# Kernel optimization log

Measured on AMD Instinct MI355X. Metric: run time of the kernel, lower is better.

## Reference

```python
import jax, jax.numpy as jnp
import numpy as np

N_NODES = 50000
C = 128
E = 800000
B = 4096
NEG = 5
NUM_LAYERS = 3


def setup_inputs() -> dict:
    key = jax.random.key(0)
    ks = jax.random.split(key, 8)
    edge_index = jax.random.randint(ks[0], (2, E), 0, N_NODES, dtype=jnp.int64)
    edge_weight = jax.random.uniform(ks[1], (E,), dtype=jnp.float32)
    n_id = jax.random.randint(ks[2], ((2 + NEG) * B,), 0, N_NODES, dtype=jnp.int64)
    x = jnp.zeros((1,), jnp.float32)  # ignored by forward (overwritten by id_embed)
    id_embed = jax.random.normal(ks[3], (N_NODES, C), jnp.float32) * 0.1
    w1 = jax.random.normal(ks[4], (2 * C, C), jnp.float32) * (1.0 / np.sqrt(2 * C))
    b1 = jnp.zeros((C,), jnp.float32)
    w2 = jax.random.normal(ks[5], (C, 1), jnp.float32) * (1.0 / np.sqrt(C))
    b2 = jnp.zeros((1,), jnp.float32)
    return {"x": x, "edge_index": edge_index, "edge_weight": edge_weight,
            "n_id": n_id, "neg_sample_num": NEG, "id_embed": id_embed,
            "w1": w1, "b1": b1, "w2": w2, "b2": b2}


def reference(x, edge_index, edge_weight, n_id, neg_sample_num, id_embed, w1, b1, w2, b2):
    n_nodes = id_embed.shape[0]
    row, col = edge_index[0], edge_index[1]
    # symmetric GCN normalization (LGCConv)
    deg = jax.ops.segment_sum(jnp.ones_like(row, dtype=id_embed.dtype), row,
                              num_segments=n_nodes)
    dinv = jnp.where(deg > 0, jax.lax.rsqrt(jnp.maximum(deg, 1e-12)), 0.0)
    norm = (dinv[row] * dinv[col])[:, None]  # [E,1]
    h = id_embed
    final = id_embed
    for _ in range(NUM_LAYERS):
        h = jax.ops.segment_sum(norm * h[col], row, num_segments=n_nodes)
        final = final + h
    final = final / (NUM_LAYERS + 1)
    # split n_id into (out, pos, neg) index groups
    b = n_id.shape[0] // (2 + neg_sample_num)
    out = final[n_id[:b]]
    pos = final[n_id[b:2 * b]]
    neg = final[n_id[2 * b:]]
    tiled_out = jnp.repeat(out, neg_sample_num, axis=0)  # [b*neg, C]

    def pred_head(z):  # Linear -> LeakyReLU(0.2) -> (Dropout eval=identity) -> Linear
        z = jax.nn.leaky_relu(z @ w1 + b1, negative_slope=0.2)
        return z @ w2 + b2

    pos_logit = pred_head(jnp.concatenate([out, pos], axis=-1))
    neg_logits = pred_head(jnp.concatenate([tiled_out, neg], axis=-1))
    return pos_logit, neg_logits
```

## Files before the change

### kernel.cpp

```cpp
#include <hip/hip_runtime.h>
#include <hip/hip_bf16.h>

#define C 128
#define NBKT 128
#define BCAP 8192

typedef __bf16 bf16x8 __attribute__((ext_vector_type(8)));
typedef float floatx4 __attribute__((ext_vector_type(4)));

__device__ __forceinline__ unsigned short f2bf(float f) {
    unsigned u = __float_as_uint(f);
    unsigned r = (u + 0x7FFFu + ((u >> 16) & 1u)) >> 16;
    return (unsigned short)r;
}
__device__ __forceinline__ float bflo(unsigned v) { return __uint_as_float(v << 16); }
__device__ __forceinline__ float bfhi(unsigned v) { return __uint_as_float(v & 0xFFFF0000u); }
__device__ __forceinline__ unsigned packbf(float lo, float hi) {
    return (unsigned)f2bf(lo) | ((unsigned)f2bf(hi) << 16);
}

__device__ __forceinline__ int g_idx(const void* p, long long i, int is64) {
    if (is64) return (int)((const long long*)p)[i];
    return ((const int*)p)[i];
}
__device__ __forceinline__ float g_flt(const void* p, long long i, int isf32) {
    if (isf32) return ((const float*)p)[i];
    return __uint_as_float(((unsigned)((const unsigned short*)p)[i]) << 16);
}

__global__ void k_detect(const void* edge, const void* nid, const void* emb, int* flags,
                         unsigned* g0, unsigned* g1, unsigned* g2, int* bucketcnt,
                         int N, int SST) {
    int t = threadIdx.x;
    int buf = t >> 6, w = t & 63;
    size_t o = (size_t)(w >> 5) * SST + (size_t)N * 32 + (w & 31);
    if (buf == 0) g0[o] = 0;
    else if (buf == 1) g1[o] = 0;
    else g2[o] = 0;
    if (t < NBKT) bucketcnt[t] = 0;
    if (t < 64) {
        const unsigned* wrd = (const unsigned*)edge;
        const unsigned* nw = (const unsigned*)nid;
        int predA = (t < 32) ? (wrd[2 * t + 1] == 0u) : 1;
        int predB = (t < 32) ? (nw[2 * t + 1] == 0u) : 1;
        const unsigned short* h = (const unsigned short*)emb;
        int ex = (h[2 * t] >> 7) & 0xFF;
        int plaus = (ex >= 0x6C && ex <= 0x7F) ? 1 : 0;
        unsigned long long mA = __ballot(predA);
        unsigned long long mB = __ballot(predB);
        unsigned long long mP = __ballot(plaus);
        if (t == 0) {
            flags[0] = (mA == ~0ull) ? 1 : 0;
            flags[1] = (mB == ~0ull) ? 1 : 0;
            flags[2] = (__popcll(mP) < 32) ? 1 : 0;
        }
    }
}

__global__ void k_bucketA(const void* edge, int E, int rpb, const int* flags,
                          unsigned* __restrict__ bucketbuf, int* __restrict__ bucketcnt) {
    __shared__ int lcnt[NBKT];
    __shared__ int lbase[NBKT];
    int t = threadIdx.x;
    int is64 = flags[0];
    const int PER = 8;
    int chunkSz = blockDim.x * PER;
    long long stride = (long long)gridDim.x * chunkSz;
    for (long long base = (long long)blockIdx.x * chunkSz; base < E; base += stride) {
        if (t < NBKT) lcnt[t] = 0;
        __syncthreads();
        int bkt[PER], rank[PER];
        unsigned enc[PER];
        long long e0 = base + (long long)t * PER;
        int rr[PER], cc[PER];
        if (e0 + PER <= E) {
            if (is64) {
                const long long* pr = (const long long*)edge + e0;
                const long long* pc = (const long long*)edge + E + e0;
#pragma unroll
                for (int j = 0; j < PER; j += 2) {
                    longlong2 vr = *(const longlong2*)(pr + j);
                    longlong2 vc = *(const longlong2*)(pc + j);
                    rr[j] = (int)vr.x; rr[j + 1] = (int)vr.y;
                    cc[j] = (int)vc.x; cc[j + 1] = (int)vc.y;
                }
            } else {
                const int* pr = (const int*)edge + e0;
                const int* pc = (const int*)edge + E + e0;
#pragma unroll
                for (int j = 0; j < PER; j += 4) {
                    int4 vr = *(const int4*)(pr + j);
                    int4 vc = *(const int4*)(pc + j);
                    rr[j] = vr.x; rr[j + 1] = vr.y; rr[j + 2] = vr.z; rr[j + 3] = vr.w;
                    cc[j] = vc.x; cc[j + 1] = vc.y; cc[j + 2] = vc.z; cc[j + 3] = vc.w;
                }
            }
#pragma unroll
            for (int j = 0; j < PER; ++j) {
                int b = rr[j] / rpb;
                bkt[j] = b;
                enc[j] = ((unsigned)(rr[j] - b * rpb) << 16) | (unsigned)(cc[j] & 0xFFFF);
                rank[j] = atomicAdd(&lcnt[b], 1);
            }
        } else {
#pragma unroll
            for (int j = 0; j < PER; ++j) {
                long long e = e0 + j;
                if (e < E) {
                    int r = g_idx(edge, e, is64);
                    int c = g_idx(edge, (long long)E + e, is64);
                    int b = r / rpb;
                    bkt[j] = b;
                    enc[j] = ((unsigned)(r - b * rpb) << 16) | (unsigned)(c & 0xFFFF);
                    rank[j] = atomicAdd(&lcnt[b], 1);
                } else bkt[j] = -1;
            }
        }
        __syncthreads();
        if (t < NBKT) lbase[t] = atomicAdd(&bucketcnt[t], lcnt[t]);
        __syncthreads();
#pragma unroll
        for (int j = 0; j < PER; ++j) {
            if (bkt[j] >= 0) {
                int pos = lbase[bkt[j]] + rank[j];
                if (pos < BCAP)
                    bucketbuf[(size_t)bkt[j] * BCAP + pos] = enc[j];
            }
        }
    }
}

__global__ __launch_bounds__(512) void k_bsort(
        const unsigned* __restrict__ bucketbuf, const int* __restrict__ bucketcnt,
        int* __restrict__ rowptr, float* __restrict__ dinv, float* __restrict__ di2,
        float* __restrict__ rdinv, unsigned short* __restrict__ cols16, int N, int rpb) {
    __shared__ int hist[512];
    int b = blockIdx.x;
    int t = threadIdx.x;
    int base = 0, cnt = 0, total = 0;
    for (int i = 0; i < NBKT; ++i) {
        int v = bucketcnt[i];
        if (v > BCAP) v = BCAP;
        if (i < b) base += v;
        if (i == b) cnt = v;
        total += v;
    }
    int r0 = b * rpb;
    int rows = N - r0;
    if (rows > rpb) rows = rpb;
    if (rows < 0) rows = 0;

    hist[t] = 0;
    __syncthreads();
    const unsigned* buf = bucketbuf + (size_t)b * BCAP;
    for (int i = t; i < cnt; i += 512) atomicAdd(&hist[buf[i] >> 16], 1);
    __syncthreads();
    int v = hist[t];
    __syncthreads();
    for (int off = 1; off < 512; off <<= 1) {
        int x = (t >= off) ? hist[t - off] : 0;
        __syncthreads();
        hist[t] += x;
        __syncthreads();
    }
    int excl = hist[t] - v;
    if (t < rows) {
        int r = r0 + t;
        rowptr[r] = base + excl;
        float fd = (float)v;
        float dv = (v > 0) ? rsqrtf(fd) : 0.0f;
        dinv[r] = dv;
        di2[r] = dv * dv;
        rdinv[r] = (v > 0) ? sqrtf(fd) : 0.0f;
    }
    if (b == NBKT - 1 && t == 0) rowptr[N] = total;
    __syncthreads();
    hist[t] = base + excl;
    __syncthreads();
    for (int i = t; i < cnt; i += 512) {
        unsigned u = buf[i];
        int pos = atomicAdd(&hist[u >> 16], 1);
        cols16[pos] = (unsigned short)(u & 0xFFFF);
    }
}

__global__ void k_initprep(const void* emb, const float* __restrict__ dinv,
                           unsigned* __restrict__ h0, unsigned* __restrict__ g0,
                           int n2, int SST,
                           const void* w1, const void* b1, const void* w2, const void* b2,
                           unsigned short* __restrict__ w1t, float* __restrict__ b1f,
                           float* __restrict__ w2f, float* __restrict__ b2f, const int* flags) {
    int i = blockIdx.x * blockDim.x + threadIdx.x;
    int f32 = flags[2];
    if (i < n2) {
        float lo = g_flt(emb, 2LL * i, f32);
        float hi = g_flt(emb, 2LL * i + 1, f32);
        int n = i >> 6, w = i & 63;
        size_t o = (size_t)(w >> 5) * SST + (size_t)n * 32 + (w & 31);
        h0[o] = packbf(lo, hi);
        float dv = dinv[n];
        g0[o] = packbf(lo * dv, hi * dv);
    }
    if (i < 256 * 128) {
        int k = i >> 7, n = i & 127;
        w1t[n * 256 + k] = f2bf(g_flt(w1, i, f32));
    }
    if (i < 128) {
        b1f[i] = g_flt(b1, i, f32);
        w2f[i] = g_flt(w2, i, f32);
    }
    if (i == 0) b2f[0] = g_flt(b2, 0, f32);
}

__global__ void k_layer(const int* __restrict__ rowptr, const unsigned short* __restrict__ cols16,
                        const uint4* __restrict__ gin, uint4* __restrict__ gout,
                        const float* __restrict__ di2, int N, int SSTU4) {
    int slice = blockIdx.x & 1;
    int node = (blockIdx.x >> 1) * 32 + (threadIdx.x >> 3);
    if (node >= N) return;
    int l8 = threadIdx.x & 7;
    const uint4* gs = gin + (size_t)slice * SSTU4;
    int p = rowptr[node];
    int end = rowptr[node + 1];
    float a0 = 0.f, a1 = 0.f, a2 = 0.f, a3 = 0.f;
    float a4 = 0.f, a5 = 0.f, a6 = 0.f, a7 = 0.f;
    for (int base = p; base < end; base += 8) {
        int c[8];
#pragma unroll
        for (int j = 0; j < 8; ++j) {
            int idx = base + j;
            int cv = cols16[idx];
            c[j] = (idx < end) ? cv : N;
        }
#pragma unroll
        for (int j = 0; j < 8; ++j) {
            uint4 v = gs[(size_t)c[j] * 8 + l8];
            a0 += bflo(v.x); a1 += bfhi(v.x);
            a2 += bflo(v.y); a3 += bfhi(v.y);
            a4 += bflo(v.z); a5 += bfhi(v.z);
            a6 += bflo(v.w); a7 += bfhi(v.w);
        }
    }
    float s = di2[node];
    uint4 o;
    o.x = packbf(a0 * s, a1 * s);
    o.y = packbf(a2 * s, a3 * s);
    o.z = packbf(a4 * s, a5 * s);
    o.w = packbf(a6 * s, a7 * s);
    gout[(size_t)slice * SSTU4 + (size_t)node * 8 + l8] = o;
}

__global__ void k_layer3(const int* __restrict__ rowptr, const unsigned short* __restrict__ cols16,
                         const uint4* __restrict__ gin , const uint4* __restrict__ h0,
                         const uint4* __restrict__ g1, uint4* __restrict__ fin,
                         const float* __restrict__ di2, const float* __restrict__ rdinv,
                         int N, int SSTU4) {
    int slice = blockIdx.x & 1;
    int node = (blockIdx.x >> 1) * 32 + (threadIdx.x >> 3);
    if (node >= N) return;
    int l8 = threadIdx.x & 7;
    size_t sb = (size_t)slice * SSTU4;
    const uint4* gs = gin + sb;
    int p = rowptr[node];
    int end = rowptr[node + 1];
    float a0 = 0.f, a1 = 0.f, a2 = 0.f, a3 = 0.f;
    float a4 = 0.f, a5 = 0.f, a6 = 0.f, a7 = 0.f;
    for (int base = p; base < end; base += 8) {
        int c[8];
#pragma unroll
        for (int j = 0; j < 8; ++j) {
            int idx = base + j;
            int cv = cols16[idx];
            c[j] = (idx < end) ? cv : N;
        }
#pragma unroll
        for (int j = 0; j < 8; ++j) {
            uint4 v = gs[(size_t)c[j] * 8 + l8];
            a0 += bflo(v.x); a1 += bfhi(v.x);
            a2 += bflo(v.y); a3 += bfhi(v.y);
            a4 += bflo(v.z); a5 += bfhi(v.z);
            a6 += bflo(v.w); a7 += bfhi(v.w);
        }
    }
    float s = di2[node];
    float rd = rdinv[node];
    size_t ro = (size_t)node * 8 + l8;
    uint4 x0 = h0[sb + ro];
    uint4 x1 = g1[sb + ro];
    uint4 x2 = gs[ro];
    uint4 o;
    o.x = packbf(0.25f * (bflo(x0.x) + rd * (bflo(x1.x) + bflo(x2.x) + s * a0)),
                 0.25f * (bfhi(x0.x) + rd * (bfhi(x1.x) + bfhi(x2.x) + s * a1)));
    o.y = packbf(0.25f * (bflo(x0.y) + rd * (bflo(x1.y) + bflo(x2.y) + s * a2)),
                 0.25f * (bfhi(x0.y) + rd * (bfhi(x1.y) + bfhi(x2.y) + s * a3)));
    o.z = packbf(0.25f * (bflo(x0.z) + rd * (bflo(x1.z) + bflo(x2.z) + s * a4)),
                 0.25f * (bfhi(x0.z) + rd * (bfhi(x1.z) + bfhi(x2.z) + s * a5)));
    o.w = packbf(0.25f * (bflo(x0.w) + rd * (bflo(x1.w) + bflo(x2.w) + s * a6)),
                 0.25f * (bfhi(x0.w) + rd * (bfhi(x1.w) + bfhi(x2.w) + s * a7)));
    fin[(size_t)node * 16 + slice * 8 + l8] = o;
}

__global__ void k_head(const uint4* __restrict__ fin, const void* n_id,
                       const unsigned short* __restrict__ w1t,
                       const float* __restrict__ b1f, const float* __restrict__ w2f,
                       const float* __restrict__ b2f,
                       float* __restrict__ out, int B, int NEG, const int* flags) {
    __shared__ unsigned short z[64][264];
    int t = threadIdx.x;
    int id64 = flags[1];
    int mbase = blockIdx.x * 64;

#pragma unroll
    for (int i = 0; i < 8; ++i) {
        int flat = i * 256 + t;
        int m = flat >> 5;
        int q = flat & 31;
        int gm = mbase + m;
        int r;
        if (gm < B) {
            r = (q < 16) ? g_idx(n_id, gm, id64) : g_idx(n_id, B + gm, id64);
        } else {
            int j = gm - B;
            r = (q < 16) ? g_idx(n_id, j / NEG, id64) : g_idx(n_id, 2 * B + j, id64);
        }
        uint4 v = fin[(size_t)r * 16 + (q & 15)];
        *(uint4*)((char*)&z[m][0] + q * 16) = v;
    }
    __syncthreads();

    int wave = t >> 6, lane = t & 63;
    int quad = lane >> 4, l16 = lane & 15;

    floatx4 acc[8] = {};
    bf16x8 a[8];
    const unsigned short* zrow = &z[wave * 16 + l16][0];
#pragma unroll
    for (int ks = 0; ks < 8; ++ks)
        a[ks] = *(const bf16x8*)(zrow + ks * 32 + quad * 8);

#pragma unroll
    for (int ks = 0; ks < 8; ++ks) {
#pragma unroll
        for (int nt = 0; nt < 8; ++nt) {
            bf16x8 b = *(const bf16x8*)(w1t + (nt * 16 + l16) * 256 + ks * 32 + quad * 8);
            acc[nt] = __builtin_amdgcn_mfma_f32_16x16x32_bf16(a[ks], b, acc[nt], 0, 0, 0);
        }
    }

    float s0 = 0.f, s1 = 0.f, s2 = 0.f, s3 = 0.f;
#pragma unroll
    for (int nt = 0; nt < 8; ++nt) {
        int col = nt * 16 + l16;
        float bb = b1f[col], ww = w2f[col];
        float v0 = acc[nt][0] + bb; v0 = (v0 > 0.f) ? v0 : 0.2f * v0; s0 += v0 * ww;
        float v1 = acc[nt][1] + bb; v1 = (v1 > 0.f) ? v1 : 0.2f * v1; s1 += v1 * ww;
        float v2 = acc[nt][2] + bb; v2 = (v2 > 0.f) ? v2 : 0.2f * v2; s2 += v2 * ww;
        float v3 = acc[nt][3] + bb; v3 = (v3 > 0.f) ? v3 : 0.2f * v3; s3 += v3 * ww;
    }
#pragma unroll
    for (int off = 1; off <= 8; off <<= 1) {
        s0 += __shfl_xor(s0, off, 64);
        s1 += __shfl_xor(s1, off, 64);
        s2 += __shfl_xor(s2, off, 64);
        s3 += __shfl_xor(s3, off, 64);
    }
    if (l16 == 0) {
        int rowbase = mbase + wave * 16 + quad * 4;
        float bb2 = b2f[0];
        out[rowbase + 0] = s0 + bb2;
        out[rowbase + 1] = s1 + bb2;
        out[rowbase + 2] = s2 + bb2;
        out[rowbase + 3] = s3 + bb2;
    }
}

extern "C" void kernel_launch(void* const* d_in, const int* in_sizes, int n_in,
                              void* d_out, int out_size, void* d_ws, size_t ws_size,
                              hipStream_t stream) {
    const void* edge_index = d_in[1];
    const void* n_id       = d_in[3];
    const void* id_embed   = d_in[5];
    const void* w1 = d_in[6];
    const void* b1 = d_in[7];
    const void* w2 = d_in[8];
    const void* b2 = d_in[9];
    float* out = (float*)d_out;

    const int E  = in_sizes[1] / 2;
    const int N  = in_sizes[5] / C;
    const int NEG = 5;
    const int B  = in_sizes[3] / (2 + NEG);
    const int n_out_rows = B + B * NEG;
    const int SST = (N + 1) * 32;
    const int SSTU4 = (N + 1) * 8;
    const int NB = 2 * SST;
    const int rpb = (N + NBKT - 1) / NBKT;

    size_t off = 0;
    auto alloc = [&](size_t nf) {
        char* p = (char*)d_ws + off * 4;
        off += (nf + 255) & ~(size_t)255;
        return p;
    };
    int*   flags     = (int*)alloc(8);
    int*   bucketcnt = (int*)alloc(NBKT);
    float* dinv      = (float*)alloc(N);
    float* di2       = (float*)alloc(N);
    float* rdinv     = (float*)alloc(N);
    int*   rowptr    = (int*)alloc(N + 1);
    unsigned short* cols16 = (unsigned short*)alloc(((size_t)E + 16 + 1) / 2);
    unsigned* bucketbuf = (unsigned*)alloc((size_t)NBKT * BCAP);
    unsigned* h0     = (unsigned*)alloc(NB);
    unsigned* g0     = (unsigned*)alloc(NB);
    unsigned* g1     = (unsigned*)alloc(NB);
    unsigned* g2     = (unsigned*)alloc(NB);
    unsigned* fin    = (unsigned*)alloc((size_t)N * 64);
    unsigned short* w1t = (unsigned short*)alloc(256 * 128 / 2);
    float* b1f       = (float*)alloc(C);
    float* w2f       = (float*)alloc(C);
    float* b2f       = (float*)alloc(8);

    const int BS = 256;
    k_detect<<<1, 192, 0, stream>>>(edge_index, n_id, id_embed, flags, g0, g1, g2,
                                    bucketcnt, N, SST);
    const int gridA = (E + BS * 8 - 1) / (BS * 8);
    k_bucketA<<<gridA, BS, 0, stream>>>(edge_index, E, rpb, flags, bucketbuf, bucketcnt);
    k_bsort<<<NBKT, 512, 0, stream>>>(bucketbuf, bucketcnt, rowptr, dinv, di2, rdinv,
                                      cols16, N, rpb);
    k_initprep<<<(N * 64 + BS - 1) / BS, BS, 0, stream>>>(
        id_embed, dinv, h0, g0, N * 64, SST, w1, b1, w2, b2, w1t, b1f, w2f, b2f, flags);

    const int layer_grid = ((N + 31) / 32) * 2;
    k_layer<<<layer_grid, BS, 0, stream>>>(rowptr, cols16, (const uint4*)g0, (uint4*)g1,
                                           di2, N, SSTU4);
    k_layer<<<layer_grid, BS, 0, stream>>>(rowptr, cols16, (const uint4*)g1, (uint4*)g2,
                                           di2, N, SSTU4);
    k_layer3<<<layer_grid, BS, 0, stream>>>(rowptr, cols16, (const uint4*)g2, (const uint4*)h0,
                                            (const uint4*)g1, (uint4*)fin, di2, rdinv,
                                            N, SSTU4);

    k_head<<<n_out_rows / 64, BS, 0, stream>>>((const uint4*)fin, n_id, w1t, b1f, w2f, b2f,
                                               out, B, NEG, flags);
}
```

Measured before the change: 216.0 us.

## Fuse init and three propagation layers into a cooperative persistent kernel

Replaces the separate init-prep and three per-layer launches with one cooperative persistent kernel that uses grid-wide syncs between phases, with a multi-launch fallback. The first layer now applies the per-column dinv scale inside the gather instead of storing a pre-scaled g0, so g0 is gone. Features move from a two-slice layout to a contiguous 256-byte row, gathered by 16 lanes per node. The detect kernel is dropped in favour of per-block dtype detection plus a memset. This cuts launch gaps and one full-size buffer write, but grid syncs and the reduced occupancy of a persistent grid may slow the bandwidth-bound gathers.

```diff
diff --git a/kernel.cpp b/kernel.cpp
--- a/kernel.cpp
+++ b/kernel.cpp
@@ -1,5 +1,8 @@
 #include <hip/hip_runtime.h>
 #include <hip/hip_bf16.h>
+#include <hip/hip_cooperative_groups.h>
+
+namespace cg = cooperative_groups;
 
 #define C 128
 #define NBKT 128
@@ -28,41 +31,20 @@
     return __uint_as_float(((unsigned)((const unsigned short*)p)[i]) << 16);
 }
 
-__global__ void k_detect(const void* edge, const void* nid, const void* emb, int* flags,
-                         unsigned* g0, unsigned* g1, unsigned* g2, int* bucketcnt,
-                         int N, int SST) {
-    int t = threadIdx.x;
-    int buf = t >> 6, w = t & 63;
-    size_t o = (size_t)(w >> 5) * SST + (size_t)N * 32 + (w & 31);
-    if (buf == 0) g0[o] = 0;
-    else if (buf == 1) g1[o] = 0;
-    else g2[o] = 0;
-    if (t < NBKT) bucketcnt[t] = 0;
-    if (t < 64) {
-        const unsigned* wrd = (const unsigned*)edge;
-        const unsigned* nw = (const unsigned*)nid;
-        int predA = (t < 32) ? (wrd[2 * t + 1] == 0u) : 1;
-        int predB = (t < 32) ? (nw[2 * t + 1] == 0u) : 1;
-        const unsigned short* h = (const unsigned short*)emb;
-        int ex = (h[2 * t] >> 7) & 0xFF;
-        int plaus = (ex >= 0x6C && ex <= 0x7F) ? 1 : 0;
-        unsigned long long mA = __ballot(predA);
-        unsigned long long mB = __ballot(predB);
-        unsigned long long mP = __ballot(plaus);
-        if (t == 0) {
-            flags[0] = (mA == ~0ull) ? 1 : 0;
-            flags[1] = (mB == ~0ull) ? 1 : 0;
-            flags[2] = (__popcll(mP) < 32) ? 1 : 0;
-        }
-    }
-}
-
-__global__ void k_bucketA(const void* edge, int E, int rpb, const int* flags,
+__global__ void k_bucketA(const void* edge, int E, int rpb,
                           unsigned* __restrict__ bucketbuf, int* __restrict__ bucketcnt) {
     __shared__ int lcnt[NBKT];
     __shared__ int lbase[NBKT];
+    __shared__ int sflag;
     int t = threadIdx.x;
-    int is64 = flags[0];
+    if (t < 64) {
+        const unsigned* wrd = (const unsigned*)edge;
+        int predA = (t < 32) ? (wrd[2 * t + 1] == 0u) : 1;
+        unsigned long long mA = __ballot(predA);
+        if (t == 0) sflag = (mA == ~0ull) ? 1 : 0;
+    }
+    __syncthreads();
+    int is64 = sflag;
     const int PER = 8;
     int chunkSz = blockDim.x * PER;
     long long stride = (long long)gridDim.x * chunkSz;
@@ -184,130 +166,184 @@
     }
 }
 
-__global__ void k_initprep(const void* emb, const float* __restrict__ dinv,
-                           unsigned* __restrict__ h0, unsigned* __restrict__ g0,
-                           int n2, int SST,
-                           const void* w1, const void* b1, const void* w2, const void* b2,
-                           unsigned short* __restrict__ w1t, float* __restrict__ b1f,
-                           float* __restrict__ w2f, float* __restrict__ b2f, const int* flags) {
-    int i = blockIdx.x * blockDim.x + threadIdx.x;
-    int f32 = flags[2];
-    if (i < n2) {
-        float lo = g_flt(emb, 2LL * i, f32);
-        float hi = g_flt(emb, 2LL * i + 1, f32);
-        int n = i >> 6, w = i & 63;
-        size_t o = (size_t)(w >> 5) * SST + (size_t)n * 32 + (w & 31);
-        h0[o] = packbf(lo, hi);
-        float dv = dinv[n];
-        g0[o] = packbf(lo * dv, hi * dv);
-    }
-    if (i < 256 * 128) {
-        int k = i >> 7, n = i & 127;
-        w1t[n * 256 + k] = f2bf(g_flt(w1, i, f32));
-    }
-    if (i < 128) {
-        b1f[i] = g_flt(b1, i, f32);
-        w2f[i] = g_flt(w2, i, f32);
-    }
-    if (i == 0) b2f[0] = g_flt(b2, 0, f32);
-}
-
-__global__ void k_layer(const int* __restrict__ rowptr, const unsigned short* __restrict__ cols16,
-                        const uint4* __restrict__ gin, uint4* __restrict__ gout,
-                        const float* __restrict__ di2, int N, int SSTU4) {
-    int slice = blockIdx.x & 1;
-    int node = (blockIdx.x >> 1) * 32 + (threadIdx.x >> 3);
-    if (node >= N) return;
-    int l8 = threadIdx.x & 7;
-    const uint4* gs = gin + (size_t)slice * SSTU4;
-    int p = rowptr[node];
-    int end = rowptr[node + 1];
-    float a0 = 0.f, a1 = 0.f, a2 = 0.f, a3 = 0.f;
-    float a4 = 0.f, a5 = 0.f, a6 = 0.f, a7 = 0.f;
-    for (int base = p; base < end; base += 8) {
-        int c[8];
-#pragma unroll
-        for (int j = 0; j < 8; ++j) {
-            int idx = base + j;
-            int cv = cols16[idx];
-            c[j] = (idx < end) ? cv : N;
+struct CoopArgs {
+    const void* emb;
+    const void* w1; const void* b1; const void* w2; const void* b2;
+    const int* rowptr; const unsigned short* cols16;
+    float* dinv; float* di2; float* rdinv;
+    unsigned* h0; unsigned* g1; unsigned* g2; unsigned* fin;
+    unsigned short* w1t; float* b1f; float* w2f; float* b2f;
+    int N;
+};
+
+__device__ __forceinline__ void phase0_body(const CoopArgs& a, int f32, int bid, int nblk, int t) {
+    long long gid = (long long)bid * 256 + t;
+    long long stride = (long long)nblk * 256;
+    int N = a.N;
+    long long n64 = (long long)N * 64;
+    for (long long i = gid; i < n64; i += stride) {
+        int w = (int)(i & 63);
+        long long n = i >> 6;
+        float lo = g_flt(a.emb, n * 128 + 2 * w, f32);
+        float hi = g_flt(a.emb, n * 128 + 2 * w + 1, f32);
+        a.h0[i] = packbf(lo, hi);
+    }
+    for (long long i = gid; i < 256 * 128; i += stride) {
+        int k = (int)(i >> 7), n = (int)(i & 127);
+        a.w1t[n * 256 + k] = f2bf(g_flt(a.w1, i, f32));
+    }
+    if (gid < 128) {
+        a.b1f[(int)gid] = g_flt(a.b1, gid, f32);
+        a.w2f[(int)gid] = g_flt(a.w2, gid, f32);
+    } else if (gid == 128) {
+        a.b2f[0] = g_flt(a.b2, 0, f32);
+    } else if (gid >= 256 && gid < 320) {
+        a.h0[(size_t)N * 64 + (int)(gid - 256)] = 0u;
+    } else if (gid >= 320 && gid < 384) {
+        a.g1[(size_t)N * 64 + (int)(gid - 320)] = 0u;
+    } else if (gid >= 384 && gid < 448) {
+        a.g2[(size_t)N * 64 + (int)(gid - 384)] = 0u;
+    } else if (gid == 448) {
+        a.dinv[N] = 0.f; a.di2[N] = 0.f; a.rdinv[N] = 0.f;
+    }
+}
+
+template<bool SC, bool L3M>
+__device__ __forceinline__ void layer_body(
+        const int* __restrict__ rowptr, const unsigned short* __restrict__ cols16,
+        const uint4* __restrict__ gin, uint4* __restrict__ gout,
+        const float* __restrict__ dsc, const float* __restrict__ di2,
+        const float* __restrict__ rdinv,
+        const uint4* __restrict__ h0, const uint4* __restrict__ g1,
+        int N, int bid, int nblk, int t) {
+    int l16 = t & 15;
+    int nsub = t >> 4;
+    for (int nb = bid; nb * 16 < N; nb += nblk) {
+        int node = nb * 16 + nsub;
+        if (node < N) {
+            int p = rowptr[node], end = rowptr[node + 1];
+            float a0 = 0.f, a1 = 0.f, a2 = 0.f, a3 = 0.f;
+            float a4 = 0.f, a5 = 0.f, a6 = 0.f, a7 = 0.f;
+            for (int base = p; base < end; base += 8) {
+                int c[8];
+#pragma unroll
+                for (int j = 0; j < 8; ++j) {
+                    int idx = base + j;
+                    int cv = cols16[idx];
+                    c[j] = (idx < end) ? cv : N;
+                }
+#pragma unroll
+                for (int j = 0; j < 8; ++j) {
+                    uint4 v = gin[(size_t)c[j] * 16 + l16];
+                    if (SC) {
+                        float dc = dsc[c[j]];
+                        a0 = fmaf(dc, bflo(v.x), a0); a1 = fmaf(dc, bfhi(v.x), a1);
+                        a2 = fmaf(dc, bflo(v.y), a2); a3 = fmaf(dc, bfhi(v.y), a3);
+                        a4 = fmaf(dc, bflo(v.z), a4); a5 = fmaf(dc, bfhi(v.z), a5);
+                        a6 = fmaf(dc, bflo(v.w), a6); a7 = fmaf(dc, bfhi(v.w), a7);
+                    } else {
+                        a0 += bflo(v.x); a1 += bfhi(v.x);
+                        a2 += bflo(v.y); a3 += bfhi(v.y);
+                        a4 += bflo(v.z); a5 += bfhi(v.z);
+                        a6 += bflo(v.w); a7 += bfhi(v.w);
+                    }
+                }
+            }
+            float s = di2[node];
+            size_t ro = (size_t)node * 16 + l16;
+            uint4 o;
+            if (!L3M) {
+                o.x = packbf(a0 * s, a1 * s);
+                o.y = packbf(a2 * s, a3 * s);
+                o.z = packbf(a4 * s, a5 * s);
+                o.w = packbf(a6 * s, a7 * s);
+            } else {
+                float rd = rdinv[node];
+                uint4 x0 = h0[ro];
+                uint4 x1 = g1[ro];
+                uint4 x2 = gin[ro];
+                o.x = packbf(0.25f * (bflo(x0.x) + rd * (bflo(x1.x) + bflo(x2.x) + s * a0)),
+                             0.25f * (bfhi(x0.x) + rd * (bfhi(x1.x) + bfhi(x2.x) + s * a1)));
+                o.y = packbf(0.25f * (bflo(x0.y) + rd * (bflo(x1.y) + bflo(x2.y) + s * a2)),
+                             0.25f * (bfhi(x0.y) + rd * (bfhi(x1.y) + bfhi(x2.y) + s * a3)));
+                o.z = packbf(0.25f * (bflo(x0.z) + rd * (bflo(x1.z) + bflo(x2.z) + s * a4)),
+                             0.25f * (bfhi(x0.z) + rd * (bfhi(x1.z) + bfhi(x2.z) + s * a5)));
+                o.w = packbf(0.25f * (bflo(x0.w) + rd * (bflo(x1.w) + bflo(x2.w) + s * a6)),
+                             0.25f * (bfhi(x0.w) + rd * (bfhi(x1.w) + bfhi(x2.w) + s * a7)));
+            }
+            gout[ro] = o;
         }
-#pragma unroll
-        for (int j = 0; j < 8; ++j) {
-            uint4 v = gs[(size_t)c[j] * 8 + l8];
-            a0 += bflo(v.x); a1 += bfhi(v.x);
-            a2 += bflo(v.y); a3 += bfhi(v.y);
-            a4 += bflo(v.z); a5 += bfhi(v.z);
-            a6 += bflo(v.w); a7 += bfhi(v.w);
-        }
-    }
-    float s = di2[node];
-    uint4 o;
-    o.x = packbf(a0 * s, a1 * s);
-    o.y = packbf(a2 * s, a3 * s);
-    o.z = packbf(a4 * s, a5 * s);
-    o.w = packbf(a6 * s, a7 * s);
-    gout[(size_t)slice * SSTU4 + (size_t)node * 8 + l8] = o;
-}
-
-__global__ void k_layer3(const int* __restrict__ rowptr, const unsigned short* __restrict__ cols16,
-                         const uint4* __restrict__ gin , const uint4* __restrict__ h0,
-                         const uint4* __restrict__ g1, uint4* __restrict__ fin,
-                         const float* __restrict__ di2, const float* __restrict__ rdinv,
-                         int N, int SSTU4) {
-    int slice = blockIdx.x & 1;
-    int node = (blockIdx.x >> 1) * 32 + (threadIdx.x >> 3);
-    if (node >= N) return;
-    int l8 = threadIdx.x & 7;
-    size_t sb = (size_t)slice * SSTU4;
-    const uint4* gs = gin + sb;
-    int p = rowptr[node];
-    int end = rowptr[node + 1];
-    float a0 = 0.f, a1 = 0.f, a2 = 0.f, a3 = 0.f;
-    float a4 = 0.f, a5 = 0.f, a6 = 0.f, a7 = 0.f;
-    for (int base = p; base < end; base += 8) {
-        int c[8];
-#pragma unroll
-        for (int j = 0; j < 8; ++j) {
-            int idx = base + j;
-            int cv = cols16[idx];
-            c[j] = (idx < end) ? cv : N;
-        }
-#pragma unroll
-        for (int j = 0; j < 8; ++j) {
-            uint4 v = gs[(size_t)c[j] * 8 + l8];
-            a0 += bflo(v.x); a1 += bfhi(v.x);
-            a2 += bflo(v.y); a3 += bfhi(v.y);
-            a4 += bflo(v.z); a5 += bfhi(v.z);
-            a6 += bflo(v.w); a7 += bfhi(v.w);
-        }
-    }
-    float s = di2[node];
-    float rd = rdinv[node];
-    size_t ro = (size_t)node * 8 + l8;
-    uint4 x0 = h0[sb + ro];
-    uint4 x1 = g1[sb + ro];
-    uint4 x2 = gs[ro];
-    uint4 o;
-    o.x = packbf(0.25f * (bflo(x0.x) + rd * (bflo(x1.x) + bflo(x2.x) + s * a0)),
-                 0.25f * (bfhi(x0.x) + rd * (bfhi(x1.x) + bfhi(x2.x) + s * a1)));
-    o.y = packbf(0.25f * (bflo(x0.y) + rd * (bflo(x1.y) + bflo(x2.y) + s * a2)),
-                 0.25f * (bfhi(x0.y) + rd * (bfhi(x1.y) + bfhi(x2.y) + s * a3)));
-    o.z = packbf(0.25f * (bflo(x0.z) + rd * (bflo(x1.z) + bflo(x2.z) + s * a4)),
-                 0.25f * (bfhi(x0.z) + rd * (bfhi(x1.z) + bfhi(x2.z) + s * a5)));
-    o.w = packbf(0.25f * (bflo(x0.w) + rd * (bflo(x1.w) + bflo(x2.w) + s * a6)),
-                 0.25f * (bfhi(x0.w) + rd * (bfhi(x1.w) + bfhi(x2.w) + s * a7)));
-    fin[(size_t)node * 16 + slice * 8 + l8] = o;
+    }
+}
+
+__device__ __forceinline__ int detect_f32(const void* emb, int t, int* sm) {
+    if (t < 64) {
+        const unsigned short* h = (const unsigned short*)emb;
+        int ex = (h[2 * t] >> 7) & 0xFF;
+        unsigned long long mP = __ballot(ex >= 0x6C && ex <= 0x7F);
+        if (t == 0) *sm = (__popcll(mP) < 32) ? 1 : 0;
+    }
+    __syncthreads();
+    return *sm;
+}
+
+__global__ __launch_bounds__(256) void k_coop(CoopArgs a) {
+    cg::grid_group grid = cg::this_grid();
+    __shared__ int sf32;
+    int t = threadIdx.x;
+    int bid = blockIdx.x, nblk = gridDim.x;
+    int f32 = detect_f32(a.emb, t, &sf32);
+    phase0_body(a, f32, bid, nblk, t);
+    grid.sync();
+    layer_body<true, false>(a.rowptr, a.cols16, (const uint4*)a.h0, (uint4*)a.g1,
+                            a.dinv, a.di2, nullptr, nullptr, nullptr, a.N, bid, nblk, t);
+    grid.sync();
+    layer_body<false, false>(a.rowptr, a.cols16, (const uint4*)a.g1, (uint4*)a.g2,
+                             nullptr, a.di2, nullptr, nullptr, nullptr, a.N, bid, nblk, t);
+    grid.sync();
+    layer_body<false, true>(a.rowptr, a.cols16, (const uint4*)a.g2, (uint4*)a.fin,
+                            nullptr, a.di2, a.rdinv, (const uint4*)a.h0, (const uint4*)a.g1,
+                            a.N, bid, nblk, t);
+}
+
+__global__ __launch_bounds__(256) void k_p0(CoopArgs a) {
+    __shared__ int sf32;
+    int t = threadIdx.x;
+    int f32 = detect_f32(a.emb, t, &sf32);
+    phase0_body(a, f32, blockIdx.x, gridDim.x, t);
+}
+__global__ __launch_bounds__(256) void k_l1(CoopArgs a) {
+    layer_body<true, false>(a.rowptr, a.cols16, (const uint4*)a.h0, (uint4*)a.g1,
+                            a.dinv, a.di2, nullptr, nullptr, nullptr, a.N,
+                            blockIdx.x, gridDim.x, threadIdx.x);
+}
+__global__ __launch_bounds__(256) void k_l2(CoopArgs a) {
+    layer_body<false, false>(a.rowptr, a.cols16, (const uint4*)a.g1, (uint4*)a.g2,
+                             nullptr, a.di2, nullptr, nullptr, nullptr, a.N,
+                             blockIdx.x, gridDim.x, threadIdx.x);
+}
+__global__ __launch_bounds__(256) void k_l3(CoopArgs a) {
+    layer_body<false, true>(a.rowptr, a.cols16, (const uint4*)a.g2, (uint4*)a.fin,
+                            nullptr, a.di2, a.rdinv, (const uint4*)a.h0, (const uint4*)a.g1,
+                            a.N, blockIdx.x, gridDim.x, threadIdx.x);
 }
 
 __global__ void k_head(const uint4* __restrict__ fin, const void* n_id,
                        const unsigned short* __restrict__ w1t,
                        const float* __restrict__ b1f, const float* __restrict__ w2f,
                        const float* __restrict__ b2f,
-                       float* __restrict__ out, int B, int NEG, const int* flags) {
+                       float* __restrict__ out, int B, int NEG) {
     __shared__ unsigned short z[64][264];
+    __shared__ int sid;
     int t = threadIdx.x;
-    int id64 = flags[1];
+    if (t < 64) {
+        const unsigned* nw = (const unsigned*)n_id;
+        int predB = (t < 32) ? (nw[2 * t + 1] == 0u) : 1;
+        unsigned long long mB = __ballot(predB);
+        if (t == 0) sid = (mB == ~0ull) ? 1 : 0;
+    }
+    __syncthreads();
+    int id64 = sid;
     int mbase = blockIdx.x * 64;
 
 #pragma unroll
@@ -391,9 +427,6 @@
     const int NEG = 5;
     const int B  = in_sizes[3] / (2 + NEG);
     const int n_out_rows = B + B * NEG;
-    const int SST = (N + 1) * 32;
-    const int SSTU4 = (N + 1) * 8;
-    const int NB = 2 * SST;
     const int rpb = (N + NBKT - 1) / NBKT;
 
     size_t off = 0;
@@ -402,18 +435,16 @@
         off += (nf + 255) & ~(size_t)255;
         return p;
     };
-    int*   flags     = (int*)alloc(8);
     int*   bucketcnt = (int*)alloc(NBKT);
-    float* dinv      = (float*)alloc(N);
-    float* di2       = (float*)alloc(N);
-    float* rdinv     = (float*)alloc(N);
+    float* dinv      = (float*)alloc(N + 1);
+    float* di2       = (float*)alloc(N + 1);
+    float* rdinv     = (float*)alloc(N + 1);
     int*   rowptr    = (int*)alloc(N + 1);
     unsigned short* cols16 = (unsigned short*)alloc(((size_t)E + 16 + 1) / 2);
     unsigned* bucketbuf = (unsigned*)alloc((size_t)NBKT * BCAP);
-    unsigned* h0     = (unsigned*)alloc(NB);
-    unsigned* g0     = (unsigned*)alloc(NB);
-    unsigned* g1     = (unsigned*)alloc(NB);
-    unsigned* g2     = (unsigned*)alloc(NB);
+    unsigned* h0     = (unsigned*)alloc((size_t)(N + 1) * 64);
+    unsigned* g1     = (unsigned*)alloc((size_t)(N + 1) * 64);
+    unsigned* g2     = (unsigned*)alloc((size_t)(N + 1) * 64);
     unsigned* fin    = (unsigned*)alloc((size_t)N * 64);
     unsigned short* w1t = (unsigned short*)alloc(256 * 128 / 2);
     float* b1f       = (float*)alloc(C);
@@ -421,24 +452,49 @@
     float* b2f       = (float*)alloc(8);
 
     const int BS = 256;
-    k_detect<<<1, 192, 0, stream>>>(edge_index, n_id, id_embed, flags, g0, g1, g2,
-                                    bucketcnt, N, SST);
+    hipMemsetAsync(bucketcnt, 0, NBKT * sizeof(int), stream);
+
     const int gridA = (E + BS * 8 - 1) / (BS * 8);
-    k_bucketA<<<gridA, BS, 0, stream>>>(edge_index, E, rpb, flags, bucketbuf, bucketcnt);
+    k_bucketA<<<gridA, BS, 0, stream>>>(edge_index, E, rpb, bucketbuf, bucketcnt);
     k_bsort<<<NBKT, 512, 0, stream>>>(bucketbuf, bucketcnt, rowptr, dinv, di2, rdinv,
                                       cols16, N, rpb);
-    k_initprep<<<(N * 64 + BS - 1) / BS, BS, 0, stream>>>(
-        id_embed, dinv, h0, g0, N * 64, SST, w1, b1, w2, b2, w1t, b1f, w2f, b2f, flags);
-
-    const int layer_grid = ((N + 31) / 32) * 2;
-    k_layer<<<layer_grid, BS, 0, stream>>>(rowptr, cols16, (const uint4*)g0, (uint4*)g1,
-                                           di2, N, SSTU4);
-    k_layer<<<layer_grid, BS, 0, stream>>>(rowptr, cols16, (const uint4*)g1, (uint4*)g2,
-                                           di2, N, SSTU4);
-    k_layer3<<<layer_grid, BS, 0, stream>>>(rowptr, cols16, (const uint4*)g2, (const uint4*)h0,
-                                            (const uint4*)g1, (uint4*)fin, di2, rdinv,
-                                            N, SSTU4);
+
+    CoopArgs ca;
+    ca.emb = id_embed; ca.w1 = w1; ca.b1 = b1; ca.w2 = w2; ca.b2 = b2;
+    ca.rowptr = rowptr; ca.cols16 = cols16;
+    ca.dinv = dinv; ca.di2 = di2; ca.rdinv = rdinv;
+    ca.h0 = h0; ca.g1 = g1; ca.g2 = g2; ca.fin = fin;
+    ca.w1t = w1t; ca.b1f = b1f; ca.w2f = w2f; ca.b2f = b2f;
+    ca.N = N;
+
+    static int sCoopGrid = -1;
+    if (sCoopGrid < 0) {
+        int perCU = 0;
+        hipOccupancyMaxActiveBlocksPerMultiprocessor(&perCU, k_coop, BS, 0);
+        if (perCU <= 0) perCU = 2;
+        int nCU = 256;
+        hipDeviceProp_t prop;
+        int dev = 0;
+        if (hipGetDevice(&dev) == hipSuccess &&
+            hipGetDeviceProperties(&prop, dev) == hipSuccess &&
+            prop.multiProcessorCount > 0)
+            nCU = prop.multiProcessorCount;
+        sCoopGrid = perCU * nCU;
+    }
+    int tiles = (N + 15) / 16;
+    int coopGrid = sCoopGrid < tiles ? sCoopGrid : tiles;
+
+    void* kp[] = {&ca};
+    hipError_t cerr = hipLaunchCooperativeKernel((void*)k_coop, dim3(coopGrid), dim3(BS),
+                                                 kp, 0, stream);
+    if (cerr != hipSuccess) {
+        int g = 2048 < tiles ? 2048 : tiles;
+        k_p0<<<g, BS, 0, stream>>>(ca);
+        k_l1<<<g, BS, 0, stream>>>(ca);
+        k_l2<<<g, BS, 0, stream>>>(ca);
+        k_l3<<<g, BS, 0, stream>>>(ca);
+    }
 
     k_head<<<n_out_rows / 64, BS, 0, stream>>>((const uint4*)fin, n_id, w1t, b1f, w2f, b2f,
-                                               out, B, NEG, flags);
-}
+                                               out, B, NEG);
+}
```

After: 458.3 us. 112% more time.
